# Performance work log

Hardware: AMD Instinct MI355X
Metric: run time of the kernel (lower is better)

The kernel has to match this reference:

```python
import jax, jax.numpy as jnp
import numpy as np

B, L, HID, LOW = 1024, 64, 512, 20
TEMP = 1.0
EPS = 1e-20


def setup_inputs() -> dict:
    key = jax.random.key(0)
    ks = jax.random.split(key, 8)
    input_h = jax.random.normal(ks[0], (B, L, HID), jnp.float32)
    input_c = jax.random.normal(ks[1], (B, L, HID), jnp.float32)
    length = jax.random.randint(ks[2], (B,), L // 2, L + 1)          # valid lengths in [L/2, L]
    u_noise = jax.random.uniform(ks[3], (L - 1, B, L - 1), jnp.float32)  # gumbel uniforms per level
    s = 1.0 / np.sqrt(HID)
    W_reduce = jax.random.uniform(ks[4], (HID, LOW), jnp.float32, -s, s)
    b_reduce = jnp.zeros((LOW,), jnp.float32)
    s2 = 1.0 / np.sqrt(2 * LOW)
    W_comp = jax.random.uniform(ks[5], (2 * LOW, 5 * LOW), jnp.float32, -s2, s2)
    b_comp = jnp.zeros((5 * LOW,), jnp.float32)
    query = jax.random.normal(ks[6], (LOW,), jnp.float32) / np.sqrt(LOW)
    return dict(input_h=input_h, input_c=input_c, W_reduce=W_reduce, b_reduce=b_reduce,
                W_comp=W_comp, b_comp=b_comp, query=query, u_noise=u_noise, length=length)


def _treelstm(hl, cl, hr, cr, W, b):
    # BinaryTreeLSTMLayer.forward: concat children, one Linear to 5 gates
    v = jnp.concatenate([hl, hr], axis=-1) @ W + b          # (B, n, 5*LOW)
    i_, fl, fr, u_, o = jnp.split(v, 5, axis=-1)
    c = cl * jax.nn.sigmoid(fl + 1.0) + cr * jax.nn.sigmoid(fr + 1.0) \
        + jnp.tanh(u_) * jax.nn.sigmoid(i_)
    h = jax.nn.sigmoid(o) * jnp.tanh(c)
    return h, c


def _masked_softmax(logits, mask):
    probs = jax.nn.softmax(logits, axis=1)
    probs = probs * mask + EPS
    return probs / probs.sum(axis=1, keepdims=True)


def _st_gumbel(logits, u, mask):
    g = -jnp.log(-jnp.log(u + EPS) + EPS)                   # gumbel noise (non-diff, matches .data)
    y = _masked_softmax((logits + g) / TEMP, mask)
    y_hard = jax.nn.one_hot(jnp.argmax(y, axis=1), y.shape[1], dtype=y.dtype)
    return jax.lax.stop_gradient(y_hard - y) + y            # straight-through


def _forward(input_h, input_c, W_reduce, b_reduce, W_comp, b_comp, query, u_noise, length):
    h = input_h @ W_reduce + b_reduce                       # (B, L, LOW)  reduce_dim
    c = input_c @ W_reduce + b_reduce
    length_mask = (jnp.arange(L)[None, :] < length[:, None]).astype(h.dtype)  # (B, L)
    for i in range(L - 1):                                  # sequential DP over pyramid levels
        hl, cl = h[:, :-1], c[:, :-1]
        hr, cr = h[:, 1:], c[:, 1:]
        nh, nc = _treelstm(hl, cl, hr, cr, W_comp, b_comp)  # (B, L-1-i, LOW) all adjacent merges
        if i < L - 2:
            logits = nh @ query                             # dot_nd scoring, (B, L-1-i)
            sel = _st_gumbel(logits, u_noise[i, :, :L - 1 - i], length_mask[:, i + 1:])
            cum = jnp.cumsum(sel, axis=1)
            left = (1.0 - cum)[..., None]                   # keep old left spans
            right = (cum - sel)[..., None]                  # shift old right spans
            se = sel[..., None]
            nh = se * nh + left * hl + right * hr
            nc = se * nc + left * cl + right * cr
        done = length_mask[:, i + 1][:, None, None]         # update_state done_mask
        h = done * nh + (1.0 - done) * hl
        c = done * nc + (1.0 - done) * cl
    return h[:, 0]                                          # (B, LOW) root hidden state


def reference(input_h, input_c, W_reduce, b_reduce, W_comp, b_comp, query, u_noise, length):
    return _forward(input_h, input_c, W_reduce, b_reduce, W_comp, b_comp, query, u_noise, length)
```

## Files before the change

### kernel.cpp

```cpp
#include <hip/hip_runtime.h>
#include <cmath>
#include <cfloat>

namespace {

constexpr int kB   = 1024;
constexpr int kL   = 64;
constexpr int kHid = 512;
constexpr int kLow = 20;
constexpr int kLM1 = 63;
constexpr int kRowElems = kL * kLow;

__device__ __forceinline__ float fsig(float x) {
  return __builtin_amdgcn_rcpf(1.0f + __expf(-x));
}
__device__ __forceinline__ float ftanhf(float x) {
  return 1.0f - 2.0f * __builtin_amdgcn_rcpf(1.0f + __expf(2.0f * x));
}
__device__ __forceinline__ int rdl_i(int v, int l) {
  return __builtin_amdgcn_readlane(v, l);
}
__device__ __forceinline__ float rdl_f(float v, int l) {
  return __int_as_float(__builtin_amdgcn_readlane(__float_as_int(v), l));
}

#define DPPI(v, ctrl) __builtin_amdgcn_update_dpp((v), (v), (ctrl), 0xF, 0xF, false)
#define DPPF(v, ctrl) __int_as_float(DPPI(__float_as_int(v), (ctrl)))
#define DPPF0(v, ctrl)                                                        \
  __int_as_float(__builtin_amdgcn_update_dpp(0, __float_as_int(v), (ctrl),    \
                                             0xF, 0xF, true))
#define UMAX_STAGE(CTRL)                                                      \
  {                                                                           \
    const unsigned o_ = (unsigned)DPPI((int)m, CTRL);                         \
    m = (m > o_) ? m : o_;                                                    \
  }

__global__ __launch_bounds__(256, 3)
void reduce_kernel(const float* __restrict__ Xh, const float* __restrict__ Xc,
                   const float* __restrict__ W, const float* __restrict__ bv,
                   float* __restrict__ H0, float* __restrict__ C0) {
  __shared__ float xs[64 * 132];
  __shared__ float wsm[128 * 20];

  const int bid = blockIdx.x;
  const float* __restrict__ X = (bid < kB) ? Xh : Xc;
  float* __restrict__ O       = (bid < kB) ? H0 : C0;
  const int b = bid & (kB - 1);
  X += (size_t)b * kL * kHid;
  O += (size_t)b * kRowElems;

  const int tid  = threadIdx.x;
  const int wave = tid >> 6;
  const int lane = tid & 63;

  float acc[20];
#pragma unroll
  for (int d = 0; d < 20; ++d) acc[d] = 0.0f;

  for (int ch = 0; ch < 4; ++ch) {
    __syncthreads();
#pragma unroll
    for (int r = 0; r < 8; ++r) {
      int f   = r * 256 + tid;
      int row = f >> 5;
      int c4  = (f & 31) << 2;
      float4 v = *(const float4*)(X + row * kHid + ch * 128 + c4);
      *(float4*)(xs + row * 132 + c4) = v;
    }
#pragma unroll
    for (int r = 0; r < 10; ++r) {
      int f = r * 256 + tid;
      wsm[f] = W[ch * 2560 + f];
    }
    __syncthreads();
#pragma unroll
    for (int kk = 0; kk < 32; ++kk) {
      int k = wave * 32 + kk;
      float x = xs[lane * 132 + k];
      const float4* wp = (const float4*)(wsm + k * 20);
      float4 w0 = wp[0], w1 = wp[1], w2 = wp[2], w3 = wp[3], w4 = wp[4];
      acc[0]  = fmaf(x, w0.x, acc[0]);  acc[1]  = fmaf(x, w0.y, acc[1]);
      acc[2]  = fmaf(x, w0.z, acc[2]);  acc[3]  = fmaf(x, w0.w, acc[3]);
      acc[4]  = fmaf(x, w1.x, acc[4]);  acc[5]  = fmaf(x, w1.y, acc[5]);
      acc[6]  = fmaf(x, w1.z, acc[6]);  acc[7]  = fmaf(x, w1.w, acc[7]);
      acc[8]  = fmaf(x, w2.x, acc[8]);  acc[9]  = fmaf(x, w2.y, acc[9]);
      acc[10] = fmaf(x, w2.z, acc[10]); acc[11] = fmaf(x, w2.w, acc[11]);
      acc[12] = fmaf(x, w3.x, acc[12]); acc[13] = fmaf(x, w3.y, acc[13]);
      acc[14] = fmaf(x, w3.z, acc[14]); acc[15] = fmaf(x, w3.w, acc[15]);
      acc[16] = fmaf(x, w4.x, acc[16]); acc[17] = fmaf(x, w4.y, acc[17]);
      acc[18] = fmaf(x, w4.z, acc[18]); acc[19] = fmaf(x, w4.w, acc[19]);
    }
  }

  __syncthreads();
  float* red = xs;
#pragma unroll
  for (int d = 0; d < 20; ++d) red[wave * 1280 + lane * 20 + d] = acc[d];
  __syncthreads();
#pragma unroll
  for (int r = 0; r < 5; ++r) {
    int f = r * 256 + tid;
    float s = (red[f] + red[1280 + f]) + (red[2560 + f] + red[3840 + f]);
    O[f] = s + bv[f % 20];
  }
}

#define EVAL_UNIT(A_, B2_, PS_, DD_, HN_)                                     \
  {                                                                           \
    float ai = bcs[DD_], af = bcs[20 + DD_], ag = bcs[40 + DD_],              \
          au = bcs[60 + DD_], ao = bcs[80 + DD_];                             \
    const int xa_ = (A_)*20, xb_ = (B2_)*20, wr_ = (DD_)*44;                  \
    _Pragma("unroll")                                                         \
    for (int kq = 0; kq < 10; ++kq) {                                         \
      const float4 xq = (kq < 5)                                              \
          ? *(const float4*)(h_state + xa_ + kq * 4)                          \
          : *(const float4*)(h_state + xb_ + (kq - 5) * 4);                   \
      const float4 wi = *(const float4*)(Wt + wr_ + kq * 4);                  \
      const float4 wf = *(const float4*)(Wt + 880  + wr_ + kq * 4);           \
      const float4 wg = *(const float4*)(Wt + 1760 + wr_ + kq * 4);           \
      const float4 wu = *(const float4*)(Wt + 2640 + wr_ + kq * 4);           \
      const float4 wo = *(const float4*)(Wt + 3520 + wr_ + kq * 4);           \
      ai = fmaf(xq.x, wi.x, ai); ai = fmaf(xq.y, wi.y, ai);                   \
      ai = fmaf(xq.z, wi.z, ai); ai = fmaf(xq.w, wi.w, ai);                   \
      af = fmaf(xq.x, wf.x, af); af = fmaf(xq.y, wf.y, af);                   \
      af = fmaf(xq.z, wf.z, af); af = fmaf(xq.w, wf.w, af);                   \
      ag = fmaf(xq.x, wg.x, ag); ag = fmaf(xq.y, wg.y, ag);                   \
      ag = fmaf(xq.z, wg.z, ag); ag = fmaf(xq.w, wg.w, ag);                   \
      au = fmaf(xq.x, wu.x, au); au = fmaf(xq.y, wu.y, au);                   \
      au = fmaf(xq.z, wu.z, au); au = fmaf(xq.w, wu.w, au);                   \
      ao = fmaf(xq.x, wo.x, ao); ao = fmaf(xq.y, wo.y, ao);                   \
      ao = fmaf(xq.z, wo.z, ao); ao = fmaf(xq.w, wo.w, ao);                   \
    }                                                                         \
    const float cl_ = c_state[(A_)*20 + (DD_)],                               \
                cr_ = c_state[(B2_)*20 + (DD_)];                              \
    const float cn_ = cl_ * fsig(af + 1.0f) + cr_ * fsig(ag + 1.0f) +         \
                      ftanhf(au) * fsig(ai);                                  \
    (HN_) = fsig(ao) * ftanhf(cn_);                                           \
    nh[(PS_)*20 + (DD_)] = (HN_);                                             \
    nc[(PS_)*20 + (DD_)] = cn_;                                               \
  }

#define EVAL_KS(PXA_, PXB_, PCL_, PCR_, HN_, CN_)                             \
  {                                                                           \
    const float* xp_ = half ? (PXB_) : (PXA_);                                \
    float xr_[20];                                                            \
    _Pragma("unroll")                                                         \
    for (int q_ = 0; q_ < 5; ++q_) {                                          \
      const float4 t_ = *(const float4*)(xp_ + q_ * 4);                       \
      xr_[q_*4+0]=t_.x; xr_[q_*4+1]=t_.y; xr_[q_*4+2]=t_.z; xr_[q_*4+3]=t_.w; \
    }                                                                         \
    float si_=0.f, sfl_=0.f, sfr_=0.f, su_=0.f, so_=0.f;                      \
    _Pragma("unroll")                                                         \
    for (int kk_ = 0; kk_ < 20; ++kk_) {                                      \
      si_  = fmaf(xr_[kk_], w0[kk_], si_);                                    \
      sfl_ = fmaf(xr_[kk_], w1[kk_], sfl_);                                   \
      sfr_ = fmaf(xr_[kk_], w2[kk_], sfr_);                                   \
      su_  = fmaf(xr_[kk_], w3[kk_], su_);                                    \
      so_  = fmaf(xr_[kk_], w4[kk_], so_);                                    \
    }                                                                         \
    si_  += __shfl_xor(si_, 32);                                              \
    sfl_ += __shfl_xor(sfl_, 32);                                             \
    sfr_ += __shfl_xor(sfr_, 32);                                             \
    su_  += __shfl_xor(su_, 32);                                              \
    so_  += __shfl_xor(so_, 32);                                              \
    si_ += bi; sfl_ += bfl; sfr_ += bfr; su_ += bu; so_ += bo;                \
    const float cl_ = (PCL_)[ddc];                                            \
    const float cr_ = (PCR_)[ddc];                                            \
    (CN_) = cl_ * fsig(sfl_ + 1.0f) + cr_ * fsig(sfr_ + 1.0f) +               \
            ftanhf(su_) * fsig(si_);                                          \
    (HN_) = fsig(so_) * ftanhf(CN_);                                          \
  }

__global__ __launch_bounds__(64, 1)
void pyramid_kernel(const float* __restrict__ H0, const float* __restrict__ C0,
                    const float* __restrict__ Wc, const float* __restrict__ bcg,
                    const float* __restrict__ query, const float* __restrict__ U,
                    const int* __restrict__ length, float* __restrict__ out) {
  __shared__ float h_state[64 * 20];
  __shared__ float c_state[64 * 20];
  __shared__ float nh[63 * 20];
  __shared__ float nc[63 * 20];
  __shared__ float Wt[100 * 44];
  __shared__ float bcs[100];
  __shared__ float qvs[20];

  const int b    = blockIdx.x;
  const int lane = threadIdx.x;
  const int half = lane >> 5;
  const int dd   = lane & 31;
  const int ddc  = dd < 20 ? dd : 19;
  int len = length[b];
  len = len < 1 ? 1 : (len > 64 ? 64 : len);

  {
    const float4* h4 = (const float4*)(H0 + (size_t)b * kRowElems);
    const float4* c4 = (const float4*)(C0 + (size_t)b * kRowElems);
#pragma unroll
    for (int r = 0; r < 5; ++r) {
      int f = r * 64 + lane;
      ((float4*)h_state)[f] = h4[f];
      ((float4*)c_state)[f] = c4[f];
    }
  }
  for (int f = lane; f < 4000; f += 64) {
    int c = f / 40, k = f - c * 40;
    Wt[c * 44 + k] = Wc[k * 100 + c];
  }
  for (int f = lane; f < 100; f += 64) bcs[f] = bcg[f];
  if (lane < 20) qvs[lane] = query[lane];

  int   idx_r  = lane;
  int   pidx_r = lane;
  float lgt_r  = -FLT_MAX;

  const int col = lane < 62 ? lane : 62;
  const float u_row0 = U[b * kLM1 + col];
  float u_c = (kLM1 > 1) ? U[1 * (kB * kLM1) + b * kLM1 + col] : 0.0f;

#pragma unroll 1
  for (int r = 0; r < 20; ++r) {
    int uu = r * 64 + lane;
    if (uu < 1260) {
      int p = uu / 20, d2 = uu - p * 20;
      float hn_;
      EVAL_UNIT(p, p + 1, p, d2, hn_);
      (void)hn_;
    }
  }
  if (lane < 63) {
    float s = 0.0f;
#pragma unroll
    for (int q = 0; q < 5; ++q) {
      const float4 t  = *(const float4*)(nh  + lane * 20 + q * 4);
      const float4 qv = *(const float4*)(qvs + q * 4);
      s = fmaf(t.x, qv.x, s); s = fmaf(t.y, qv.y, s);
      s = fmaf(t.z, qv.z, s); s = fmaf(t.w, qv.w, s);
    }
    lgt_r = s;
  }

  float w0[20], w1[20], w2[20], w3[20], w4[20];
#pragma unroll
  for (int q = 0; q < 5; ++q) {
    float4 t;
    t = *(const float4*)(Wt + (0  + ddc) * 44 + half * 20 + q * 4);
    w0[q*4+0]=t.x; w0[q*4+1]=t.y; w0[q*4+2]=t.z; w0[q*4+3]=t.w;
    t = *(const float4*)(Wt + (20 + ddc) * 44 + half * 20 + q * 4);
    w1[q*4+0]=t.x; w1[q*4+1]=t.y; w1[q*4+2]=t.z; w1[q*4+3]=t.w;
    t = *(const float4*)(Wt + (40 + ddc) * 44 + half * 20 + q * 4);
    w2[q*4+0]=t.x; w2[q*4+1]=t.y; w2[q*4+2]=t.z; w2[q*4+3]=t.w;
    t = *(const float4*)(Wt + (60 + ddc) * 44 + half * 20 + q * 4);
    w3[q*4+0]=t.x; w3[q*4+1]=t.y; w3[q*4+2]=t.z; w3[q*4+3]=t.w;
    t = *(const float4*)(Wt + (80 + ddc) * 44 + half * 20 + q * 4);
    w4[q*4+0]=t.x; w4[q*4+1]=t.y; w4[q*4+2]=t.z; w4[q*4+3]=t.w;
  }
#pragma unroll
  for (int j = 0; j < 20; ++j) {
    asm volatile("" : "+v"(w0[j]), "+v"(w1[j]), "+v"(w2[j]),
                      "+v"(w3[j]), "+v"(w4[j]));
  }
  const float bi  = bcs[ddc],      bfl = bcs[20 + ddc], bfr = bcs[40 + ddc],
              bu  = bcs[60 + ddc], bo  = bcs[80 + ddc];
  const float qq  = qvs[ddc];

  float gcur = -__logf(-__logf(u_row0 + 1e-20f) + 1e-20f);

  const int nIter = len - 1;
#pragma unroll 1
  for (int i = 0; i < nIter; ++i) {
    const int n = kL - i;

    const float zf = lgt_r + gcur;
    const unsigned ub  = __float_as_uint(zf);
    unsigned key = ((int)ub < 0) ? ~ub : (ub | 0x80000000u);
    const bool valid = (lane <= n - 2) && ((i + 1 + lane) < len);
    if (!valid) key = 0u;
    unsigned m = key;
    UMAX_STAGE(0xB1);
    UMAX_STAGE(0x4E);
    UMAX_STAGE(0x141);
    UMAX_STAGE(0x140);
    UMAX_STAGE(0x142);
    UMAX_STAGE(0x143);
    const unsigned gmax = (unsigned)rdl_i((int)m, 63);
    const unsigned long long bal = __ballot(valid && (key == gmax));
    const int k = (int)(__ffsll(bal) - 1);

    float u_d = 0.0f;
    if (i + 2 <= kLM1 - 1) u_d = U[(i + 2) * (kB * kLM1) + b * kLM1 + col];

    const int km1 = (k >= 1) ? k - 1 : 0;
    const int kp2 = (k <= n - 3) ? k + 2 : 0;
    const int tgt = rdl_i(idx_r,  k);
    const int psk = rdl_i(pidx_r, k);
    const int iA  = rdl_i(idx_r,  km1);
    const int pA  = rdl_i(pidx_r, km1);
    const int iB  = rdl_i(idx_r,  kp2);

    if (lane < 20) {
      h_state[tgt * 20 + lane] = nh[psk * 20 + lane];
      c_state[tgt * 20 + lane] = nc[psk * 20 + lane];
    }

    {
      int   sI = DPPI(idx_r,  0x101);
      int   sP = DPPI(pidx_r, 0x101);
      float sL = DPPF(lgt_r,  0x101);
      const int   bi16 = rdl_i(idx_r, 16),  bi32 = rdl_i(idx_r, 32),
                  bi48 = rdl_i(idx_r, 48);
      const int   bp16 = rdl_i(pidx_r, 16), bp32 = rdl_i(pidx_r, 32),
                  bp48 = rdl_i(pidx_r, 48);
      const float bl16 = rdl_f(lgt_r, 16),  bl32 = rdl_f(lgt_r, 32),
                  bl48 = rdl_f(lgt_r, 48);
      if (lane == 15) { sI = bi16; sP = bp16; sL = bl16; }
      if (lane == 31) { sI = bi32; sP = bp32; sL = bl32; }
      if (lane == 47) { sI = bi48; sP = bp48; sL = bl48; }
      const bool doI = (lane >= k + 1) && (lane <= n - 2);
      const bool doP = (lane >= k + 1) && (lane <= n - 3);
      if (doI) idx_r = sI;
      if (doP) { pidx_r = sP; lgt_r = sL; }
    }

    if (i < len - 2) {
      const bool hasA = (k >= 1);
      const bool hasB = (k <= n - 3);
      float hnA, cnA, hnB, cnB;
      EVAL_KS(h_state + iA * 20, nh + psk * 20,
              c_state + iA * 20, nc + psk * 20, hnA, cnA);
      EVAL_KS(nh + psk * 20, h_state + iB * 20,
              nc + psk * 20, c_state + iB * 20, hnB, cnB);
      if (hasA && half == 0 && dd < 20) {
        nh[pA * 20 + dd] = hnA;  nc[pA * 20 + dd] = cnA;
      }
      if (hasB && half == 1 && dd < 20) {
        nh[psk * 20 + dd] = hnB; nc[psk * 20 + dd] = cnB;
      }
      float pr = 0.0f;
      if (dd < 20) pr = half ? hnB * qq : hnA * qq;
      pr += DPPF0(pr, 0xB1);
      pr += DPPF0(pr, 0x4E);
      pr += DPPF0(pr, 0x141);
      pr += DPPF0(pr, 0x140);
      pr += DPPF0(pr, 0x142);
      const float vA = rdl_f(pr, 31);
      const float vB = rdl_f(pr, 63);
      if (hasA && lane == k - 1) lgt_r = vA;
      if (hasB && lane == k)     lgt_r = vB;
    }

    gcur = -__logf(-__logf(u_c + 1e-20f) + 1e-20f);
    u_c  = u_d;
  }

  const int root = rdl_i(idx_r, 0);
  if (lane < 20) {
    out[b * 20 + lane] = h_state[root * 20 + lane];
  }
}

}

extern "C" void kernel_launch(void* const* d_in, const int* in_sizes, int n_in,
                              void* d_out, int out_size, void* d_ws, size_t ws_size,
                              hipStream_t stream) {
  const float* input_h  = (const float*)d_in[0];
  const float* input_c  = (const float*)d_in[1];
  const float* W_reduce = (const float*)d_in[2];
  const float* b_reduce = (const float*)d_in[3];
  const float* W_comp   = (const float*)d_in[4];
  const float* b_comp   = (const float*)d_in[5];
  const float* query    = (const float*)d_in[6];
  const float* u_noise  = (const float*)d_in[7];
  const int*   length   = (const int*)d_in[8];
  float* out = (float*)d_out;

  float* H0 = (float*)d_ws;
  float* C0 = H0 + (size_t)kB * kL * kLow;

  reduce_kernel<<<dim3(2 * kB), dim3(256), 0, stream>>>(
      input_h, input_c, W_reduce, b_reduce, H0, C0);
  pyramid_kernel<<<dim3(kB), dim3(64), 0, stream>>>(
      H0, C0, W_comp, b_comp, query, u_noise, length, out);
}
```

Measured before the change: 174.9 us.

## Halve reduce-kernel LDS chunks for occupancy; use packed FMA in pyramid gate eval

The reduce kernel now stages 64-column chunks instead of 128, with a padded stride of 65, and raises the launch bound to 6 blocks per CU. This cuts LDS per block so more blocks can be resident. In the pyramid kernel, the per-step gate dot products now use v_pk_fma_f32 on float2 pairs, halving the FMA instruction count, followed by a final horizontal add. The asm volatile pins that kept the weights in registers are removed, so the compiler may allocate them differently.

```diff
diff --git a/kernel.cpp b/kernel.cpp
--- a/kernel.cpp
+++ b/kernel.cpp
@@ -10,6 +10,8 @@
 constexpr int kLow = 20;
 constexpr int kLM1 = 63;
 constexpr int kRowElems = kL * kLow;
+
+typedef float v2f __attribute__((ext_vector_type(2)));
 
 __device__ __forceinline__ float fsig(float x) {
   return __builtin_amdgcn_rcpf(1.0f + __expf(-x));
@@ -35,12 +37,15 @@
     m = (m > o_) ? m : o_;                                                    \
   }
 
-__global__ __launch_bounds__(256, 3)
+#define PKFMA(ACC, X, W)                                                      \
+  asm("v_pk_fma_f32 %0, %1, %2, %0" : "+v"(ACC) : "v"(X), "v"(W))
+
+__global__ __launch_bounds__(256, 6)
 void reduce_kernel(const float* __restrict__ Xh, const float* __restrict__ Xc,
                    const float* __restrict__ W, const float* __restrict__ bv,
                    float* __restrict__ H0, float* __restrict__ C0) {
-  __shared__ float xs[64 * 132];
-  __shared__ float wsm[128 * 20];
+  __shared__ float xs[5184];
+  __shared__ float wsm[64 * 20];
 
   const int bid = blockIdx.x;
   const float* __restrict__ X = (bid < kB) ? Xh : Xc;
@@ -57,26 +62,26 @@
 #pragma unroll
   for (int d = 0; d < 20; ++d) acc[d] = 0.0f;
 
-  for (int ch = 0; ch < 4; ++ch) {
+  for (int ch = 0; ch < 8; ++ch) {
     __syncthreads();
 #pragma unroll
-    for (int r = 0; r < 8; ++r) {
+    for (int r = 0; r < 4; ++r) {
       int f   = r * 256 + tid;
-      int row = f >> 5;
-      int c4  = (f & 31) << 2;
-      float4 v = *(const float4*)(X + row * kHid + ch * 128 + c4);
-      *(float4*)(xs + row * 132 + c4) = v;
-    }
-#pragma unroll
-    for (int r = 0; r < 10; ++r) {
+      int row = f >> 4;
+      int c4  = (f & 15) << 2;
+      float4 v = *(const float4*)(X + row * kHid + ch * 64 + c4);
+      *(float4*)(xs + row * 65 + c4) = v;
+    }
+#pragma unroll
+    for (int r = 0; r < 5; ++r) {
       int f = r * 256 + tid;
-      wsm[f] = W[ch * 2560 + f];
+      wsm[f] = W[ch * 1280 + f];
     }
     __syncthreads();
 #pragma unroll
-    for (int kk = 0; kk < 32; ++kk) {
-      int k = wave * 32 + kk;
-      float x = xs[lane * 132 + k];
+    for (int kk = 0; kk < 16; ++kk) {
+      int k = wave * 16 + kk;
+      float x = xs[lane * 65 + k];
       const float4* wp = (const float4*)(wsm + k * 20);
       float4 w0 = wp[0], w1 = wp[1], w2 = wp[2], w3 = wp[3], w4 = wp[4];
       acc[0]  = fmaf(x, w0.x, acc[0]);  acc[1]  = fmaf(x, w0.y, acc[1]);
@@ -143,21 +148,25 @@
 #define EVAL_KS(PXA_, PXB_, PCL_, PCR_, HN_, CN_)                             \
   {                                                                           \
     const float* xp_ = half ? (PXB_) : (PXA_);                                \
-    float xr_[20];                                                            \
+    v2f x2_[10];                                                              \
     _Pragma("unroll")                                                         \
     for (int q_ = 0; q_ < 5; ++q_) {                                          \
       const float4 t_ = *(const float4*)(xp_ + q_ * 4);                       \
-      xr_[q_*4+0]=t_.x; xr_[q_*4+1]=t_.y; xr_[q_*4+2]=t_.z; xr_[q_*4+3]=t_.w; \
+      x2_[q_*2+0] = (v2f){t_.x, t_.y};                                        \
+      x2_[q_*2+1] = (v2f){t_.z, t_.w};                                        \
     }                                                                         \
-    float si_=0.f, sfl_=0.f, sfr_=0.f, su_=0.f, so_=0.f;                      \
+    v2f a0_ = (v2f){0.f,0.f}, a1_ = a0_, a2_ = a0_, a3_ = a0_, a4_ = a0_;     \
     _Pragma("unroll")                                                         \
-    for (int kk_ = 0; kk_ < 20; ++kk_) {                                      \
-      si_  = fmaf(xr_[kk_], w0[kk_], si_);                                    \
-      sfl_ = fmaf(xr_[kk_], w1[kk_], sfl_);                                   \
-      sfr_ = fmaf(xr_[kk_], w2[kk_], sfr_);                                   \
-      su_  = fmaf(xr_[kk_], w3[kk_], su_);                                    \
-      so_  = fmaf(xr_[kk_], w4[kk_], so_);                                    \
+    for (int q_ = 0; q_ < 10; ++q_) {                                         \
+      PKFMA(a0_, x2_[q_], W0[q_]);                                            \
+      PKFMA(a1_, x2_[q_], W1[q_]);                                            \
+      PKFMA(a2_, x2_[q_], W2[q_]);                                            \
+      PKFMA(a3_, x2_[q_], W3[q_]);                                            \
+      PKFMA(a4_, x2_[q_], W4[q_]);                                            \
     }                                                                         \
+    float si_ = a0_[0] + a0_[1], sfl_ = a1_[0] + a1_[1],                      \
+          sfr_ = a2_[0] + a2_[1], su_ = a3_[0] + a3_[1],                      \
+          so_ = a4_[0] + a4_[1];                                              \
     si_  += __shfl_xor(si_, 32);                                              \
     sfl_ += __shfl_xor(sfl_, 32);                                             \
     sfr_ += __shfl_xor(sfr_, 32);                                             \
@@ -239,25 +248,20 @@
     lgt_r = s;
   }
 
-  float w0[20], w1[20], w2[20], w3[20], w4[20];
+  v2f W0[10], W1[10], W2[10], W3[10], W4[10];
 #pragma unroll
   for (int q = 0; q < 5; ++q) {
     float4 t;
     t = *(const float4*)(Wt + (0  + ddc) * 44 + half * 20 + q * 4);
-    w0[q*4+0]=t.x; w0[q*4+1]=t.y; w0[q*4+2]=t.z; w0[q*4+3]=t.w;
+    W0[q*2] = (v2f){t.x, t.y}; W0[q*2+1] = (v2f){t.z, t.w};
     t = *(const float4*)(Wt + (20 + ddc) * 44 + half * 20 + q * 4);
-    w1[q*4+0]=t.x; w1[q*4+1]=t.y; w1[q*4+2]=t.z; w1[q*4+3]=t.w;
+    W1[q*2] = (v2f){t.x, t.y}; W1[q*2+1] = (v2f){t.z, t.w};
     t = *(const float4*)(Wt + (40 + ddc) * 44 + half * 20 + q * 4);
-    w2[q*4+0]=t.x; w2[q*4+1]=t.y; w2[q*4+2]=t.z; w2[q*4+3]=t.w;
+    W2[q*2] = (v2f){t.x, t.y}; W2[q*2+1] = (v2f){t.z, t.w};
     t = *(const float4*)(Wt + (60 + ddc) * 44 + half * 20 + q * 4);
-    w3[q*4+0]=t.x; w3[q*4+1]=t.y; w3[q*4+2]=t.z; w3[q*4+3]=t.w;
+    W3[q*2] = (v2f){t.x, t.y}; W3[q*2+1] = (v2f){t.z, t.w};
     t = *(const float4*)(Wt + (80 + ddc) * 44 + half * 20 + q * 4);
-    w4[q*4+0]=t.x; w4[q*4+1]=t.y; w4[q*4+2]=t.z; w4[q*4+3]=t.w;
-  }
-#pragma unroll
-  for (int j = 0; j < 20; ++j) {
-    asm volatile("" : "+v"(w0[j]), "+v"(w1[j]), "+v"(w2[j]),
-                      "+v"(w3[j]), "+v"(w4[j]));
+    W4[q*2] = (v2f){t.x, t.y}; W4[q*2+1] = (v2f){t.z, t.w};
   }
   const float bi  = bcs[ddc],      bfl = bcs[20 + ddc], bfr = bcs[40 + ddc],
               bu  = bcs[60 + ddc], bo  = bcs[80 + ddc];
```

Result: no change. 171.5 us (-2.0%).
